# Optimization experiments

Hardware: AMD Instinct MI355X
Metric: run time of the kernel (lower is better)

## Reference

```python
import jax, jax.numpy as jnp
import numpy as np

B, T, D, H, W = 2, 16, 32, 64, 64
C2 = 2 * D          # channels after real/imag concat
E4 = 4 * C2         # para_pool expand=4
EPS = 1e-5


def _cnorm(z, g, b):
    # complex 'norm': LayerNorm over concat([real, imag], -1), then recombine
    zc = jnp.concatenate([z.real, z.imag], axis=-1)
    mu = zc.mean(-1, keepdims=True)
    var = zc.var(-1, keepdims=True)
    zn = (zc - mu) / jnp.sqrt(var + EPS) * g + b
    r, i = jnp.split(zn, 2, axis=-1)
    return r + 1j * i


def setup_inputs() -> dict:
    key = jax.random.key(0)
    ks = jax.random.split(key, 16)
    f = jnp.float32
    sd = 1.0 / np.sqrt(D)
    return {
        "x_real": jax.random.normal(ks[0], (B, T, D, H, W), f),
        "x_imag": jax.random.normal(ks[1], (B, T, D, H, W), f),
        "dt": jnp.ones((1,), f),
        "ln_s_g": jnp.ones((C2,), f), "ln_s_b": jnp.zeros((C2,), f),
        "conv_w": jax.random.normal(ks[2], (3, 3, C2, C2), f) * 0.05,
        "conv_b": jnp.zeros((C2,), f),
        "spec_fr": jax.random.normal(ks[3], (H, W, D), f) * 0.1,
        "spec_fi": jax.random.normal(ks[4], (H, W, D), f) * 0.1,
        "lam_r": -jnp.abs(jax.random.normal(ks[5], (D,), f)) * 0.5,
        "lam_i": jax.random.normal(ks[6], (D,), f),
        "E_r": jax.random.normal(ks[7], (D, D), f) * sd,
        "E_i": jax.random.normal(ks[8], (D, D), f) * sd,
        "Dm_r": jax.random.normal(ks[9], (D, D), f) * sd,
        "Dm_i": jax.random.normal(ks[10], (D, D), f) * sd,
        "ln_t_g": jnp.ones((C2,), f), "ln_t_b": jnp.zeros((C2,), f),
        "pool_w1": jax.random.normal(ks[11], (E4, C2), f) * 0.05,
        "pool_b1": jnp.zeros((E4,), f),
        "pool_w2": jax.random.normal(ks[12], (C2, E4), f) * 0.05,
        "pool_b2": jnp.zeros((C2,), f),
        "gate": jnp.full((1,), 0.5, f),
    }


def reference(x_real, x_imag, dt, ln_s_g, ln_s_b, conv_w, conv_b, spec_fr, spec_fi,
              lam_r, lam_i, E_r, E_i, Dm_r, Dm_i, ln_t_g, ln_t_b,
              pool_w1, pool_b1, pool_w2, pool_b2, gate):
    # work in channel-last layout [B,T,H,W,D]
    x = (x_real + 1j * x_imag).transpose(0, 1, 3, 4, 2)

    # ---- spatial block ----
    resid = x
    zn = _cnorm(x, ln_s_g, ln_s_b)                       # [B,T,H,W,D] complex
    zc = jnp.concatenate([zn.real, zn.imag], -1).reshape(B * T, H, W, C2)
    oc = jax.lax.conv_general_dilated(
        zc, conv_w, (1, 1), 'SAME',
        dimension_numbers=('NHWC', 'HWIO', 'NHWC')) + conv_b
    r, i = jnp.split(oc.reshape(B, T, H, W, C2), 2, axis=-1)
    cliff = r + 1j * i
    filt = spec_fr + 1j * spec_fi                         # [H,W,D]
    spec = jnp.fft.ifft2(jnp.fft.fft2(zn, axes=(2, 3)) * filt, axes=(2, 3))
    g = gate[0]
    x = g * cliff + (1.0 - g) * spec + resid

    # ---- temporal block: eigen-encode -> linear-decay scan -> decode ----
    resid = x
    xt = _cnorm(x.transpose(0, 2, 3, 1, 4).reshape(B * H * W, T, D), ln_t_g, ln_t_b)
    lam = lam_r + 1j * lam_i
    dts = dt[0]
    op_decay = jnp.exp(lam * dts)                         # [D]
    op_forcing = (jnp.exp(lam * dts) - 1.0) / lam          # [D] (exact ZOH forcing)
    Em = E_r + 1j * E_i
    Dm = Dm_r + 1j * Dm_i
    x_eig = jnp.einsum('ntd,de->nte', xt, Em)
    u = x_eig * op_forcing                                # [BHW,T,D]
    a = jnp.broadcast_to(op_decay, u.shape).astype(u.dtype)

    def comb(c1, c2):
        a1, u1 = c1
        a2, u2 = c2
        return (a1 * a2, u1 * a2 + u2)

    h = jax.lax.associative_scan(comb, (a, u), axis=1)[1]  # h_t = a_t h_{t-1} + u_t
    xo = jnp.einsum('ntd,de->nte', h, Dm).real
    x_drift = xo.reshape(B, H, W, T, D).transpose(0, 3, 1, 2, 4)
    x = x_drift + resid

    # ---- para pool (pointwise channel MLP on concat(real, imag)) ----
    resid = x
    xp = jnp.concatenate([x.real, x.imag], -1)            # [B,T,H,W,2D]
    y = jax.nn.gelu(jnp.einsum('bthwc,ec->bthwe', xp, pool_w1) + pool_b1)
    y = jnp.einsum('bthwe,ce->bthwc', y, pool_w2) + pool_b2
    r, i = jnp.split(y, 2, axis=-1)
    x = (r + 1j * i) + resid

    return x.transpose(0, 1, 4, 2, 3)                     # [B,T,D,H,W] complex
```

## Files before the change

kernel.cpp:

```cpp
#include <hip/hip_runtime.h>
#include <cstddef>


#define EPS_ 1e-5f
#define PI_  3.14159265358979323846f
#define ND_  4194304ull

typedef __attribute__((ext_vector_type(8))) short bf16x8;
typedef __attribute__((ext_vector_type(4))) float f32x4;

__device__ __forceinline__ short f2bf(float f) {
  unsigned u = __float_as_uint(f);
  unsigned r = (u + 0x7fffu + ((u >> 16) & 1u)) >> 16;
  return (short)r;
}
__device__ __forceinline__ float bf2f(short h) {
  return __uint_as_float(((unsigned)(unsigned short)h) << 16);
}

__global__ __launch_bounds__(256) void k0_prepw(
    const float* __restrict__ wgt, unsigned short* __restrict__ wb) {
  int j = blockIdx.x * 256 + threadIdx.x;
  int kk = j >> 12;
  int rem = j & 4095;
  int oc = rem >> 6;
  int ic = rem & 63;
  wb[j] = (unsigned short)f2bf(wgt[((size_t)kk * 64 + ic) * 64 + oc]);
}

__global__ __launch_bounds__(256) void k8_pool_prepw(
    const float* __restrict__ pw1, const float* __restrict__ pw2,
    const float* __restrict__ Er, const float* __restrict__ Ei,
    const float* __restrict__ Dmr, const float* __restrict__ Dmi,
    unsigned short* __restrict__ pwb1, unsigned short* __restrict__ pwb2,
    unsigned short* __restrict__ eB, unsigned short* __restrict__ dB) {
  int j = blockIdx.x * 256 + threadIdx.x;
  if (j < 16384) {
    pwb1[j] = (unsigned short)f2bf(pw1[j]);
  } else if (j < 32768) {
    int j2 = j - 16384;
    int ec = j2 >> 12;
    int rem = j2 & 4095;
    int oc = rem >> 6;
    int el = rem & 63;
    pwb2[j2] = (unsigned short)f2bf(pw2[(size_t)oc * 256 + ec * 64 + el]);
  } else if (j < 36864) {
    int j2 = j - 32768;
    int col = j2 >> 6, k = j2 & 63;
    float v;
    if (col < 32) {
      v = (k < 32) ? Er[k * 32 + col] : -Ei[(k - 32) * 32 + col];
    } else {
      int e = col - 32;
      v = (k < 32) ? Ei[k * 32 + e] : Er[(k - 32) * 32 + e];
    }
    eB[j2] = (unsigned short)f2bf(v);
  } else if (j < 38912) {
    int j2 = j - 36864;
    int e2 = j2 >> 6, k = j2 & 63;
    float v = (k < 32) ? Dmr[k * 32 + e2] : -Dmi[(k - 32) * 32 + e2];
    dB[j2] = (unsigned short)f2bf(v);
  }
}

__global__ __launch_bounds__(256) void k1_cnorm_spatial(
    const float* __restrict__ xr, const float* __restrict__ xi,
    const float* __restrict__ g, const float* __restrict__ b,
    float* __restrict__ znr, float* __restrict__ zni,
    unsigned short* __restrict__ znb) {
  int tok = blockIdx.x * 256 + threadIdx.x;
  int bt = tok >> 12;
  int hw = tok & 4095;
  const float* pr = xr + (size_t)bt * 131072 + hw;
  const float* pi = xi + (size_t)bt * 131072 + hw;
  float r[32], q[32];
  float s = 0.f;
#pragma unroll
  for (int d = 0; d < 32; d++) {
    r[d] = pr[(size_t)d * 4096];
    q[d] = pi[(size_t)d * 4096];
    s += r[d] + q[d];
  }
  float mu = s * 0.015625f;
  float v = 0.f;
#pragma unroll
  for (int d = 0; d < 32; d++) {
    float a = r[d] - mu, c = q[d] - mu;
    v += a * a + c * c;
  }
  float rstd = rsqrtf(v * 0.015625f + EPS_);
#pragma unroll
  for (int d = 0; d < 32; d++) {
    r[d] = (r[d] - mu) * rstd * g[d] + b[d];
    q[d] = (q[d] - mu) * rstd * g[32 + d] + b[32 + d];
  }
  float4* outr = (float4*)(znr + (size_t)tok * 32);
  float4* outi = (float4*)(zni + (size_t)tok * 32);
#pragma unroll
  for (int j = 0; j < 8; j++) {
    outr[j] = make_float4(r[4 * j], r[4 * j + 1], r[4 * j + 2], r[4 * j + 3]);
    outi[j] = make_float4(q[4 * j], q[4 * j + 1], q[4 * j + 2], q[4 * j + 3]);
  }
  short* zb = (short*)(znb + (size_t)tok * 64);
#pragma unroll
  for (int j = 0; j < 4; j++) {
    bf16x8 vr, vq;
#pragma unroll
    for (int k = 0; k < 8; k++) {
      vr[k] = f2bf(r[8 * j + k]);
      vq[k] = f2bf(q[8 * j + k]);
    }
    *(bf16x8*)(zb + 8 * j) = vr;
    *(bf16x8*)(zb + 32 + 8 * j) = vq;
  }
}

__global__ __launch_bounds__(256) void k2_conv(
    const unsigned short* __restrict__ znb, const unsigned short* __restrict__ wb,
    const float* __restrict__ bias,
    float* __restrict__ clr, float* __restrict__ cli) {
  __shared__ __align__(16) short sA[3 * 66 * 88];
  __shared__ __align__(16) short sW[2][64 * 72];
  int h = blockIdx.x, bt = blockIdx.y;
  for (int v = threadIdx.x; v < 1584; v += 256) {
    int c0 = (v & 7) * 8;
    int row = v >> 3;
    int wp = row % 66;
    int rr = row / 66;
    int hh = h + rr - 1;
    int w = wp - 1;
    bf16x8 val = {0, 0, 0, 0, 0, 0, 0, 0};
    if ((unsigned)hh < 64u && (unsigned)w < 64u) {
      int tok = (bt * 64 + hh) * 64 + w;
      val = *(const bf16x8*)(znb + (size_t)tok * 64 + c0);
    }
    *(bf16x8*)(&sA[(rr * 66 + wp) * 88 + c0]) = val;
  }
  for (int v = threadIdx.x; v < 512; v += 256) {
    int oc = v >> 3, ic0 = (v & 7) * 8;
    *(bf16x8*)(&sW[0][oc * 72 + ic0]) = *(const bf16x8*)(wb + v * 8);
  }
  int lane = threadIdx.x & 63;
  int wv = threadIdx.x >> 6;
  int m0 = wv * 16;
  int lr = lane & 15;
  int quad = lane >> 4;
  f32x4 acc[4];
#pragma unroll
  for (int nt = 0; nt < 4; nt++) {
    float bz = bias[nt * 16 + lr];
    acc[nt][0] = bz; acc[nt][1] = bz; acc[nt][2] = bz; acc[nt][3] = bz;
  }
  __syncthreads();
  for (int kk = 0; kk < 9; kk++) {
    int cur = kk & 1;
    if (kk < 8) {
      const unsigned short* src = wb + (size_t)(kk + 1) * 4096;
      for (int v = threadIdx.x; v < 512; v += 256) {
        int oc = v >> 3, ic0 = (v & 7) * 8;
        *(bf16x8*)(&sW[cur ^ 1][oc * 72 + ic0]) = *(const bf16x8*)(src + v * 8);
      }
    }
    int kh = kk / 3, kw = kk - kh * 3;
    const short* arow = &sA[((size_t)kh * 66 + (m0 + lr + kw)) * 88 + quad * 8];
#pragma unroll
    for (int ks = 0; ks < 2; ks++) {
      bf16x8 afrag = *(const bf16x8*)(arow + ks * 32);
#pragma unroll
      for (int nt = 0; nt < 4; nt++) {
        bf16x8 bfrag = *(const bf16x8*)&sW[cur][(size_t)(nt * 16 + lr) * 72 + ks * 32 + quad * 8];
        acc[nt] = __builtin_amdgcn_mfma_f32_16x16x32_bf16(afrag, bfrag, acc[nt], 0, 0, 0);
      }
    }
    __syncthreads();
  }
  int tokbase = (bt * 64 + h) * 64 + m0;
#pragma unroll
  for (int nt = 0; nt < 4; nt++) {
    int oc = nt * 16 + lr;
    float* dst = (oc < 32) ? (clr + oc) : (cli + (oc - 32));
#pragma unroll
    for (int reg = 0; reg < 4; reg++) {
      int m = quad * 4 + reg;
      dst[(size_t)(tokbase + m) * 32] = acc[nt][reg];
    }
  }
}

__global__ __launch_bounds__(256) void k3_dftw(
    const float* __restrict__ znr, const float* __restrict__ zni,
    float* __restrict__ fqr, float* __restrict__ fqi) {
  __shared__ __align__(16) short sX[64 * 72];
  __shared__ float twr[64], twi[64];
  int h = blockIdx.x, bt = blockIdx.y;
  size_t base = (size_t)((bt * 64 + h) * 64) * 32;
  if (threadIdx.x < 64) {
    float ang = -2.f * PI_ * (float)threadIdx.x * (1.f / 64.f);
    twr[threadIdx.x] = cosf(ang);
    twi[threadIdx.x] = sinf(ang);
  }
  for (int i = threadIdx.x; i < 2048; i += 256) {
    int w = i >> 5, d = i & 31;
    sX[d * 72 + w] = f2bf(znr[base + i]);
    sX[(d + 32) * 72 + w] = f2bf(zni[base + i]);
  }
  __syncthreads();
  int lane = threadIdx.x & 63;
  int wv = threadIdx.x >> 6;
  int m0 = wv * 16;
  int lr = lane & 15;
  int quad = lane >> 4;
  int r = m0 + lr;
  bf16x8 tr0, tr1, ti0, ti1;
#pragma unroll
  for (int j = 0; j < 8; j++) {
    int i0 = (r * (quad * 8 + j)) & 63;
    int i1 = (r * (quad * 8 + j + 32)) & 63;
    tr0[j] = f2bf(twr[i0]); ti0[j] = f2bf(twi[i0]);
    tr1[j] = f2bf(twr[i1]); ti1[j] = f2bf(twi[i1]);
  }
  f32x4 p1[4], p2[4];
#pragma unroll
  for (int nt = 0; nt < 4; nt++) {
    p1[nt][0] = 0.f; p1[nt][1] = 0.f; p1[nt][2] = 0.f; p1[nt][3] = 0.f;
    p2[nt][0] = 0.f; p2[nt][1] = 0.f; p2[nt][2] = 0.f; p2[nt][3] = 0.f;
  }
#pragma unroll
  for (int ks = 0; ks < 2; ks++) {
    bf16x8 tr = ks ? tr1 : tr0;
    bf16x8 ti = ks ? ti1 : ti0;
#pragma unroll
    for (int nt = 0; nt < 4; nt++) {
      bf16x8 xh = *(const bf16x8*)&sX[(size_t)(nt * 16 + lr) * 72 + ks * 32 + quad * 8];
      p1[nt] = __builtin_amdgcn_mfma_f32_16x16x32_bf16(tr, xh, p1[nt], 0, 0, 0);
      p2[nt] = __builtin_amdgcn_mfma_f32_16x16x32_bf16(ti, xh, p2[nt], 0, 0, 0);
    }
  }
#pragma unroll
  for (int nt = 0; nt < 2; nt++) {
#pragma unroll
    for (int reg = 0; reg < 4; reg++) {
      int k = m0 + quad * 4 + reg;
      int d = nt * 16 + lr;
      float Or = p1[nt][reg] - p2[nt + 2][reg];
      float Oi = p1[nt + 2][reg] + p2[nt][reg];
      size_t la = base + (size_t)k * 32 + d;
      fqr[la] = Or;
      fqi[la] = Oi;
    }
  }
}

__global__ __launch_bounds__(256) void k4_dfth(
    float* __restrict__ fqr, float* __restrict__ fqi,
    const float* __restrict__ flr, const float* __restrict__ fli) {
  __shared__ __align__(16) short sX[64 * 72];
  __shared__ float twr[64], twi[64];
  int kw = blockIdx.x, bt = blockIdx.y;
  if (threadIdx.x < 64) {
    float ang = -2.f * PI_ * (float)threadIdx.x * (1.f / 64.f);
    twr[threadIdx.x] = cosf(ang);
    twi[threadIdx.x] = sinf(ang);
  }
  for (int i = threadIdx.x; i < 2048; i += 256) {
    int hh = i >> 5, d = i & 31;
    size_t ga = (size_t)((bt * 64 + hh) * 64 + kw) * 32 + d;
    sX[d * 72 + hh] = f2bf(fqr[ga]);
    sX[(d + 32) * 72 + hh] = f2bf(fqi[ga]);
  }
  __syncthreads();
  int lane = threadIdx.x & 63;
  int wv = threadIdx.x >> 6;
  int m0 = wv * 16;
  int lr = lane & 15;
  int quad = lane >> 4;
  int r = m0 + lr;
  bf16x8 tr0, tr1, ti0, ti1;
#pragma unroll
  for (int j = 0; j < 8; j++) {
    int i0 = (r * (quad * 8 + j)) & 63;
    int i1 = (r * (quad * 8 + j + 32)) & 63;
    tr0[j] = f2bf(twr[i0]); ti0[j] = f2bf(twi[i0]);
    tr1[j] = f2bf(twr[i1]); ti1[j] = f2bf(twi[i1]);
  }
  f32x4 p1[4], p2[4];
#pragma unroll
  for (int nt = 0; nt < 4; nt++) {
    p1[nt][0] = 0.f; p1[nt][1] = 0.f; p1[nt][2] = 0.f; p1[nt][3] = 0.f;
    p2[nt][0] = 0.f; p2[nt][1] = 0.f; p2[nt][2] = 0.f; p2[nt][3] = 0.f;
  }
#pragma unroll
  for (int ks = 0; ks < 2; ks++) {
    bf16x8 tr = ks ? tr1 : tr0;
    bf16x8 ti = ks ? ti1 : ti0;
#pragma unroll
    for (int nt = 0; nt < 4; nt++) {
      bf16x8 xh = *(const bf16x8*)&sX[(size_t)(nt * 16 + lr) * 72 + ks * 32 + quad * 8];
      p1[nt] = __builtin_amdgcn_mfma_f32_16x16x32_bf16(tr, xh, p1[nt], 0, 0, 0);
      p2[nt] = __builtin_amdgcn_mfma_f32_16x16x32_bf16(ti, xh, p2[nt], 0, 0, 0);
    }
  }
  __syncthreads();
#pragma unroll
  for (int nt = 0; nt < 2; nt++) {
#pragma unroll
    for (int reg = 0; reg < 4; reg++) {
      int kh = m0 + quad * 4 + reg;
      int d = nt * 16 + lr;
      float Or = p1[nt][reg] - p2[nt + 2][reg];
      float Oi = p1[nt + 2][reg] + p2[nt][reg];
      size_t fa = (size_t)(kh * 64 + kw) * 32 + d;
      float fr = flr[fa], fi = fli[fa];
      float pr = Or * fr - Oi * fi;
      float pi = Or * fi + Oi * fr;
      sX[d * 72 + kh] = f2bf(pr);
      sX[(d + 32) * 72 + kh] = f2bf(pi);
    }
  }
  __syncthreads();
#pragma unroll
  for (int nt = 0; nt < 4; nt++) {
    p1[nt][0] = 0.f; p1[nt][1] = 0.f; p1[nt][2] = 0.f; p1[nt][3] = 0.f;
    p2[nt][0] = 0.f; p2[nt][1] = 0.f; p2[nt][2] = 0.f; p2[nt][3] = 0.f;
  }
#pragma unroll
  for (int ks = 0; ks < 2; ks++) {
    bf16x8 tr = ks ? tr1 : tr0;
    bf16x8 ti = ks ? ti1 : ti0;
#pragma unroll
    for (int nt = 0; nt < 4; nt++) {
      bf16x8 xh = *(const bf16x8*)&sX[(size_t)(nt * 16 + lr) * 72 + ks * 32 + quad * 8];
      p1[nt] = __builtin_amdgcn_mfma_f32_16x16x32_bf16(tr, xh, p1[nt], 0, 0, 0);
      p2[nt] = __builtin_amdgcn_mfma_f32_16x16x32_bf16(ti, xh, p2[nt], 0, 0, 0);
    }
  }
#pragma unroll
  for (int nt = 0; nt < 2; nt++) {
#pragma unroll
    for (int reg = 0; reg < 4; reg++) {
      int hh = m0 + quad * 4 + reg;
      int d = nt * 16 + lr;
      float Or = (p1[nt][reg] + p2[nt + 2][reg]) * 0.015625f;
      float Oi = (p1[nt + 2][reg] - p2[nt][reg]) * 0.015625f;
      size_t ga = (size_t)((bt * 64 + hh) * 64 + kw) * 32 + d;
      fqr[ga] = Or;
      fqi[ga] = Oi;
    }
  }
}

__global__ __launch_bounds__(256) void k5_idftw_combine(
    const float* __restrict__ fqr, const float* __restrict__ fqi,
    const float* __restrict__ clr, const float* __restrict__ cli,
    const float* __restrict__ xr_in, const float* __restrict__ xi_in,
    const float* __restrict__ gate,
    float* __restrict__ xr, float* __restrict__ xi) {
  __shared__ __align__(16) short sX[64 * 72];
  __shared__ float twr[64], twi[64];
  int h = blockIdx.x, bt = blockIdx.y;
  size_t base = (size_t)((bt * 64 + h) * 64) * 32;
  if (threadIdx.x < 64) {
    float ang = -2.f * PI_ * (float)threadIdx.x * (1.f / 64.f);
    twr[threadIdx.x] = cosf(ang);
    twi[threadIdx.x] = sinf(ang);
  }
  for (int i = threadIdx.x; i < 2048; i += 256) {
    int kw = i >> 5, d = i & 31;
    sX[d * 72 + kw] = f2bf(fqr[base + i]);
    sX[(d + 32) * 72 + kw] = f2bf(fqi[base + i]);
  }
  __syncthreads();
  int lane = threadIdx.x & 63;
  int wv = threadIdx.x >> 6;
  int m0 = wv * 16;
  int lr = lane & 15;
  int quad = lane >> 4;
  int r = m0 + lr;
  bf16x8 tr0, tr1, ti0, ti1;
#pragma unroll
  for (int j = 0; j < 8; j++) {
    int i0 = (r * (quad * 8 + j)) & 63;
    int i1 = (r * (quad * 8 + j + 32)) & 63;
    tr0[j] = f2bf(twr[i0]); ti0[j] = f2bf(twi[i0]);
    tr1[j] = f2bf(twr[i1]); ti1[j] = f2bf(twi[i1]);
  }
  f32x4 p1[4], p2[4];
#pragma unroll
  for (int nt = 0; nt < 4; nt++) {
    p1[nt][0] = 0.f; p1[nt][1] = 0.f; p1[nt][2] = 0.f; p1[nt][3] = 0.f;
    p2[nt][0] = 0.f; p2[nt][1] = 0.f; p2[nt][2] = 0.f; p2[nt][3] = 0.f;
  }
#pragma unroll
  for (int ks = 0; ks < 2; ks++) {
    bf16x8 tr = ks ? tr1 : tr0;
    bf16x8 ti = ks ? ti1 : ti0;
#pragma unroll
    for (int nt = 0; nt < 4; nt++) {
      bf16x8 xh = *(const bf16x8*)&sX[(size_t)(nt * 16 + lr) * 72 + ks * 32 + quad * 8];
      p1[nt] = __builtin_amdgcn_mfma_f32_16x16x32_bf16(tr, xh, p1[nt], 0, 0, 0);
      p2[nt] = __builtin_amdgcn_mfma_f32_16x16x32_bf16(ti, xh, p2[nt], 0, 0, 0);
    }
  }
  float g = gate[0];
  float gi = 1.f - g;
#pragma unroll
  for (int nt = 0; nt < 2; nt++) {
#pragma unroll
    for (int reg = 0; reg < 4; reg++) {
      int w = m0 + quad * 4 + reg;
      int d = nt * 16 + lr;
      float Or = (p1[nt][reg] + p2[nt + 2][reg]) * 0.015625f;
      float Oi = (p1[nt + 2][reg] - p2[nt][reg]) * 0.015625f;
      size_t la = base + (size_t)w * 32 + d;
      size_t ga = (size_t)(bt * 32 + d) * 4096 + h * 64 + w;
      xr[la] = g * clr[la] + gi * Or + xr_in[ga];
      xi[la] = g * cli[la] + gi * Oi + xi_in[ga];
    }
  }
}

__global__ __launch_bounds__(256) void k6_temporal(
    float* __restrict__ xr, float* __restrict__ xi,
    const float* __restrict__ lamr, const float* __restrict__ lami,
    const unsigned short* __restrict__ eB, const unsigned short* __restrict__ dB,
    const float* __restrict__ lg, const float* __restrict__ lb,
    const float* __restrict__ dtp) {
  __shared__ __align__(16) short sAh[128 * 72];
  __shared__ __align__(16) short sAl[128 * 72];
  __shared__ __align__(16) short sBe[64 * 72];
  __shared__ __align__(16) short sBd[32 * 72];
  int n0 = blockIdx.x * 8;
  for (int v = threadIdx.x; v < 768; v += 256) {
    int c0 = (v & 7) * 8;
    if (v < 512) {
      *(bf16x8*)(&sBe[(v >> 3) * 72 + c0]) = *(const bf16x8*)(eB + v * 8);
    } else {
      int v2 = v - 512;
      *(bf16x8*)(&sBd[(v2 >> 3) * 72 + c0]) = *(const bf16x8*)(dB + v2 * 8);
    }
  }
  if (threadIdx.x < 128) {
    int sIc = threadIdx.x >> 4;
    int t = threadIdx.x & 15;
    int n = n0 + sIc;
    int bb = n >> 12;
    int hw = n & 4095;
    size_t tokb = ((size_t)(bb * 16 + t)) * 4096 + hw;
    const float4* pr = (const float4*)(xr + tokb * 32);
    const float4* pi = (const float4*)(xi + tokb * 32);
    float rv[32], iv[32];
    float s = 0.f;
#pragma unroll
    for (int j = 0; j < 8; j++) {
      float4 a = pr[j];
      float4 c = pi[j];
      rv[4 * j] = a.x; rv[4 * j + 1] = a.y; rv[4 * j + 2] = a.z; rv[4 * j + 3] = a.w;
      iv[4 * j] = c.x; iv[4 * j + 1] = c.y; iv[4 * j + 2] = c.z; iv[4 * j + 3] = c.w;
      s += a.x + a.y + a.z + a.w + c.x + c.y + c.z + c.w;
    }
    float mu = s * 0.015625f;
    float v = 0.f;
#pragma unroll
    for (int d = 0; d < 32; d++) {
      float a = rv[d] - mu, c = iv[d] - mu;
      v += a * a + c * c;
    }
    float rstd = rsqrtf(v * 0.015625f + EPS_);
    int row = threadIdx.x * 72;
#pragma unroll
    for (int j = 0; j < 4; j++) {
      bf16x8 vh, vl, wh, wl;
#pragma unroll
      for (int k = 0; k < 8; k++) {
        float a = (rv[8 * j + k] - mu) * rstd * lg[8 * j + k] + lb[8 * j + k];
        float c = (iv[8 * j + k] - mu) * rstd * lg[32 + 8 * j + k] + lb[32 + 8 * j + k];
        short ah = f2bf(a);
        vh[k] = ah; vl[k] = f2bf(a - bf2f(ah));
        short ch = f2bf(c);
        wh[k] = ch; wl[k] = f2bf(c - bf2f(ch));
      }
      *(bf16x8*)(&sAh[row + 8 * j]) = vh;
      *(bf16x8*)(&sAl[row + 8 * j]) = vl;
      *(bf16x8*)(&sAh[row + 32 + 8 * j]) = wh;
      *(bf16x8*)(&sAl[row + 32 + 8 * j]) = wl;
    }
  }
  __syncthreads();
  int lane = threadIdx.x & 63;
  int wv = threadIdx.x >> 6;
  int lr = lane & 15;
  int quad = lane >> 4;
  f32x4 p[2][4];
#pragma unroll
  for (int m = 0; m < 2; m++)
#pragma unroll
    for (int nt = 0; nt < 4; nt++) {
      p[m][nt][0] = 0.f; p[m][nt][1] = 0.f; p[m][nt][2] = 0.f; p[m][nt][3] = 0.f;
    }
#pragma unroll
  for (int m = 0; m < 2; m++) {
    int rowA = ((2 * wv + m) * 16 + lr) * 72;
#pragma unroll
    for (int ks = 0; ks < 2; ks++) {
      bf16x8 ah = *(const bf16x8*)&sAh[rowA + ks * 32 + quad * 8];
      bf16x8 al = *(const bf16x8*)&sAl[rowA + ks * 32 + quad * 8];
#pragma unroll
      for (int nt = 0; nt < 4; nt++) {
        bf16x8 bfrag = *(const bf16x8*)&sBe[(nt * 16 + lr) * 72 + ks * 32 + quad * 8];
        p[m][nt] = __builtin_amdgcn_mfma_f32_16x16x32_bf16(ah, bfrag, p[m][nt], 0, 0, 0);
        p[m][nt] = __builtin_amdgcn_mfma_f32_16x16x32_bf16(al, bfrag, p[m][nt], 0, 0, 0);
      }
    }
  }
  float dts = dtp[0];
  float acr[2], aci[2], fcr[2], fci[2];
#pragma unroll
  for (int eo = 0; eo < 2; eo++) {
    int e = eo * 16 + lr;
    float lrr = lamr[e], lii = lami[e];
    float ex = expf(lrr * dts);
    float dcr = ex * cosf(lii * dts);
    float dci = ex * sinf(lii * dts);
    acr[eo] = dcr; aci[eo] = dci;
    float nr = dcr - 1.f, ni = dci;
    float invden = 1.f / (lrr * lrr + lii * lii);
    fcr[eo] = (nr * lrr + ni * lii) * invden;
    fci[eo] = (ni * lrr - nr * lii) * invden;
  }
#pragma unroll
  for (int m = 0; m < 2; m++) {
#pragma unroll
    for (int eo = 0; eo < 2; eo++) {
      float ar = acr[eo], ai_ = aci[eo];
      float fr = fcr[eo], fi = fci[eo];
      float a2r = ar * ar - ai_ * ai_, a2i = 2.f * ar * ai_;
      float a3r = a2r * ar - a2i * ai_, a3i = a2r * ai_ + a2i * ar;
      float a4r = a2r * a2r - a2i * a2i, a4i = 2.f * a2r * a2i;
      float a8r = a4r * a4r - a4i * a4i, a8i = 2.f * a4r * a4i;
      float apr[4] = {ar, a2r, a3r, a4r};
      float api[4] = {ai_, a2i, a3i, a4i};
      float hlr[4], hli[4];
#pragma unroll
      for (int reg = 0; reg < 4; reg++) {
        float xr_ = p[m][eo][reg], xi_ = p[m][2 + eo][reg];
        float ur = xr_ * fr - xi_ * fi;
        float ui = xr_ * fi + xi_ * fr;
        if (reg == 0) {
          hlr[0] = ur; hli[0] = ui;
        } else {
          float t1 = ar * hlr[reg - 1] - ai_ * hli[reg - 1] + ur;
          float t2 = ar * hli[reg - 1] + ai_ * hlr[reg - 1] + ui;
          hlr[reg] = t1; hli[reg] = t2;
        }
      }
      float Sr = hlr[3], Si = hli[3];
      float t1r = __shfl_up(Sr, 16), t1i = __shfl_up(Si, 16);
      if (quad >= 1) { Sr += a4r * t1r - a4i * t1i; Si += a4r * t1i + a4i * t1r; }
      float t2r = __shfl_up(Sr, 32), t2i = __shfl_up(Si, 32);
      if (quad >= 2) { Sr += a8r * t2r - a8i * t2i; Si += a8r * t2i + a8i * t2r; }
      float hinr = __shfl_up(Sr, 16), hini = __shfl_up(Si, 16);
      if (quad == 0) { hinr = 0.f; hini = 0.f; }
      int e = eo * 16 + lr;
#pragma unroll
      for (int reg = 0; reg < 4; reg++) {
        float hr_ = apr[reg] * hinr - api[reg] * hini + hlr[reg];
        float hi_ = apr[reg] * hini + api[reg] * hinr + hli[reg];
        int row = ((2 * wv + m) * 16 + quad * 4 + reg) * 72;
        short b1 = f2bf(hr_);
        sAh[row + e] = b1;
        sAl[row + e] = f2bf(hr_ - bf2f(b1));
        short b2 = f2bf(hi_);
        sAh[row + 32 + e] = b2;
        sAl[row + 32 + e] = f2bf(hi_ - bf2f(b2));
      }
    }
  }
  __syncthreads();
  f32x4 q[2][2];
#pragma unroll
  for (int m = 0; m < 2; m++)
#pragma unroll
    for (int nt = 0; nt < 2; nt++) {
      q[m][nt][0] = 0.f; q[m][nt][1] = 0.f; q[m][nt][2] = 0.f; q[m][nt][3] = 0.f;
    }
#pragma unroll
  for (int m = 0; m < 2; m++) {
    int rowA = ((2 * wv + m) * 16 + lr) * 72;
#pragma unroll
    for (int ks = 0; ks < 2; ks++) {
      bf16x8 ah = *(const bf16x8*)&sAh[rowA + ks * 32 + quad * 8];
      bf16x8 al = *(const bf16x8*)&sAl[rowA + ks * 32 + quad * 8];
#pragma unroll
      for (int nt = 0; nt < 2; nt++) {
        bf16x8 bfrag = *(const bf16x8*)&sBd[(nt * 16 + lr) * 72 + ks * 32 + quad * 8];
        q[m][nt] = __builtin_amdgcn_mfma_f32_16x16x32_bf16(ah, bfrag, q[m][nt], 0, 0, 0);
        q[m][nt] = __builtin_amdgcn_mfma_f32_16x16x32_bf16(al, bfrag, q[m][nt], 0, 0, 0);
      }
    }
  }
#pragma unroll
  for (int m = 0; m < 2; m++) {
    int n = n0 + 2 * wv + m;
    int bb = n >> 12;
    int hw = n & 4095;
#pragma unroll
    for (int nt = 0; nt < 2; nt++) {
      int e2 = nt * 16 + lr;
#pragma unroll
      for (int reg = 0; reg < 4; reg++) {
        int t = quad * 4 + reg;
        size_t tokb = ((size_t)(bb * 16 + t)) * 4096 + hw;
        xr[tokb * 32 + e2] += q[m][nt][reg];
      }
    }
  }
}

__global__ __launch_bounds__(256) void k7_pool(
    const float* __restrict__ xr, const float* __restrict__ xi,
    const unsigned short* __restrict__ pwb1, const float* __restrict__ pb1,
    const unsigned short* __restrict__ pwb2, const float* __restrict__ pb2,
    float* __restrict__ out, long long out_n) {
  __shared__ __align__(16) short sX[64 * 72];
  __shared__ __align__(16) short sH[64 * 72];
  __shared__ __align__(16) short sW1[64 * 72];
  __shared__ __align__(16) short sW2[64 * 72];
  int tok0 = blockIdx.x * 64;
  for (int i = threadIdx.x; i < 4096; i += 256) {
    int t = i >> 6, c = i & 63;
    float v = (c < 32) ? xr[(size_t)(tok0 + t) * 32 + c]
                       : xi[(size_t)(tok0 + t) * 32 + c - 32];
    sX[t * 72 + c] = f2bf(v);
  }
  int lane = threadIdx.x & 63;
  int wv = threadIdx.x >> 6;
  int lr = lane & 15;
  int quad = lane >> 4;
  int m0 = wv * 16;
  f32x4 acc2[4];
#pragma unroll
  for (int nt = 0; nt < 4; nt++) {
    float bz = pb2[nt * 16 + lr];
    acc2[nt][0] = bz; acc2[nt][1] = bz; acc2[nt][2] = bz; acc2[nt][3] = bz;
  }
  const short* arow = &sX[(size_t)(m0 + lr) * 72 + quad * 8];
  const short* hrow = &sH[(size_t)(m0 + lr) * 72 + quad * 8];
  for (int ec = 0; ec < 4; ec++) {
    __syncthreads();
    {
      const unsigned short* w1 = pwb1 + (size_t)ec * 4096;
      const unsigned short* w2 = pwb2 + (size_t)ec * 4096;
      for (int v = threadIdx.x; v < 512; v += 256) {
        int row = v >> 3, c0 = (v & 7) * 8;
        *(bf16x8*)(&sW1[row * 72 + c0]) = *(const bf16x8*)(w1 + v * 8);
        *(bf16x8*)(&sW2[row * 72 + c0]) = *(const bf16x8*)(w2 + v * 8);
      }
    }
    __syncthreads();
    f32x4 acc1[4];
#pragma unroll
    for (int nt = 0; nt < 4; nt++) {
      float bz = pb1[ec * 64 + nt * 16 + lr];
      acc1[nt][0] = bz; acc1[nt][1] = bz; acc1[nt][2] = bz; acc1[nt][3] = bz;
    }
#pragma unroll
    for (int ks = 0; ks < 2; ks++) {
      bf16x8 ah = *(const bf16x8*)(arow + ks * 32);
#pragma unroll
      for (int nt = 0; nt < 4; nt++) {
        bf16x8 bfrag = *(const bf16x8*)&sW1[(size_t)(nt * 16 + lr) * 72 + ks * 32 + quad * 8];
        acc1[nt] = __builtin_amdgcn_mfma_f32_16x16x32_bf16(ah, bfrag, acc1[nt], 0, 0, 0);
      }
    }
#pragma unroll
    for (int nt = 0; nt < 4; nt++) {
#pragma unroll
      for (int reg = 0; reg < 4; reg++) {
        float x = acc1[nt][reg];
        float u2 = 1.5957691216f * (x + 0.044715f * x * x * x);
        float e2 = __expf(u2);
        float gl = x - x * __builtin_amdgcn_rcpf(e2 + 1.f);
        sH[(m0 + quad * 4 + reg) * 72 + nt * 16 + lr] = f2bf(gl);
      }
    }
#pragma unroll
    for (int ks = 0; ks < 2; ks++) {
      bf16x8 af = *(const bf16x8*)(hrow + ks * 32);
#pragma unroll
      for (int nt = 0; nt < 4; nt++) {
        bf16x8 bfrag = *(const bf16x8*)&sW2[(size_t)(nt * 16 + lr) * 72 + ks * 32 + quad * 8];
        acc2[nt] = __builtin_amdgcn_mfma_f32_16x16x32_bf16(af, bfrag, acc2[nt], 0, 0, 0);
      }
    }
  }
#pragma unroll
  for (int nt = 0; nt < 4; nt++) {
    int oc = nt * 16 + lr;
#pragma unroll
    for (int reg = 0; reg < 4; reg++) {
      int t = tok0 + m0 + quad * 4 + reg;
      float resid = (oc < 32) ? xr[(size_t)t * 32 + oc] : xi[(size_t)t * 32 + oc - 32];
      float val = acc2[nt][reg] + resid;
      int bt = t >> 12;
      int hw = t & 4095;
      int d = (oc < 32) ? oc : oc - 32;
      size_t cidx = (size_t)(bt * 32 + d) * 4096 + hw;
      long long pos = (long long)cidx + ((oc < 32) ? 0ll : (long long)ND_);
      if (pos < out_n) out[pos] = val;
    }
  }
}

extern "C" void kernel_launch(void* const* d_in, const int* in_sizes, int n_in,
                              void* d_out, int out_size, void* d_ws, size_t ws_size,
                              hipStream_t stream) {
  (void)in_sizes; (void)n_in;
  const float* xr_in = (const float*)d_in[0];
  const float* xi_in = (const float*)d_in[1];
  const float* dt = (const float*)d_in[2];
  const float* ln_s_g = (const float*)d_in[3];
  const float* ln_s_b = (const float*)d_in[4];
  const float* conv_w = (const float*)d_in[5];
  const float* conv_b = (const float*)d_in[6];
  const float* spec_fr = (const float*)d_in[7];
  const float* spec_fi = (const float*)d_in[8];
  const float* lam_r = (const float*)d_in[9];
  const float* lam_i = (const float*)d_in[10];
  const float* E_r = (const float*)d_in[11];
  const float* E_i = (const float*)d_in[12];
  const float* Dm_r = (const float*)d_in[13];
  const float* Dm_i = (const float*)d_in[14];
  const float* ln_t_g = (const float*)d_in[15];
  const float* ln_t_b = (const float*)d_in[16];
  const float* pw1 = (const float*)d_in[17];
  const float* pb1 = (const float*)d_in[18];
  const float* pw2 = (const float*)d_in[19];
  const float* pb2 = (const float*)d_in[20];
  const float* gate = (const float*)d_in[21];

  if (ws_size < 6ull * ND_ * 4ull) return;

  float* ws = (float*)d_ws;
  float* znr = ws;
  float* zni = ws + ND_;
  float* clr = ws + 2 * ND_;
  float* cli = ws + 3 * ND_;
  float* fqr = ws + 4 * ND_;
  float* fqi = ws + 5 * ND_;
  float* out = (float*)d_out;
  unsigned short* znb = (unsigned short*)fqr;
  unsigned short* wb = (unsigned short*)fqi;
  unsigned short* pwb1 = (unsigned short*)fqr;
  unsigned short* pwb2 = pwb1 + 16384;
  unsigned short* eB = pwb1 + 32768;
  unsigned short* dB = pwb1 + 36864;

  k0_prepw<<<144, 256, 0, stream>>>(conv_w, wb);
  k1_cnorm_spatial<<<512, 256, 0, stream>>>(xr_in, xi_in, ln_s_g, ln_s_b, znr, zni, znb);
  k2_conv<<<dim3(64, 32), 256, 0, stream>>>(znb, wb, conv_b, clr, cli);
  k3_dftw<<<dim3(64, 32), 256, 0, stream>>>(znr, zni, fqr, fqi);
  k4_dfth<<<dim3(64, 32), 256, 0, stream>>>(fqr, fqi, spec_fr, spec_fi);
  k5_idftw_combine<<<dim3(64, 32), 256, 0, stream>>>(fqr, fqi, clr, cli, xr_in, xi_in,
                                                     gate, znr, zni);
  k8_pool_prepw<<<156, 256, 0, stream>>>(pw1, pw2, E_r, E_i, Dm_r, Dm_i,
                                         pwb1, pwb2, eB, dB);
  k6_temporal<<<1024, 256, 0, stream>>>(znr, zni, lam_r, lam_i, eB, dB,
                                        ln_t_g, ln_t_b, dt);
  k7_pool<<<2048, 256, 0, stream>>>(znr, zni, pwb1, pb1, pwb2, pb2, out, (long long)out_size);
}
```

Baseline: 288.3 us.

## Fuse spatial cnorm with W-axis DFT and drop split-bf16 in temporal block

The spatial layernorm kernel now writes its normalized tokens as bf16 straight into shared memory and runs the W-direction DFT on four rows per block. This removes the separate DFT-W kernel and the fp32 round trip of znr/zni through global memory. Separately, the temporal kernel no longer splits activations into high and low bf16 parts, which halves its MFMA count and shared-memory use but lowers precision of the eigenbasis projections. Workspace aliasing is shuffled so the bf16 buffers reuse znr/zni.

```diff
diff --git a/kernel.cpp b/kernel.cpp
--- a/kernel.cpp
+++ b/kernel.cpp
@@ -63,14 +63,22 @@
   }
 }
 
-__global__ __launch_bounds__(256) void k1_cnorm_spatial(
+__global__ __launch_bounds__(256) void k13_cnorm_dftw(
     const float* __restrict__ xr, const float* __restrict__ xi,
     const float* __restrict__ g, const float* __restrict__ b,
-    float* __restrict__ znr, float* __restrict__ zni,
-    unsigned short* __restrict__ znb) {
-  int tok = blockIdx.x * 256 + threadIdx.x;
+    unsigned short* __restrict__ znb,
+    float* __restrict__ fqr, float* __restrict__ fqi) {
+  __shared__ __align__(16) short sX[4][64 * 72];
+  __shared__ float twr[64], twi[64];
+  int tid = threadIdx.x;
+  int tok = blockIdx.x * 256 + tid;
   int bt = tok >> 12;
   int hw = tok & 4095;
+  if (tid < 64) {
+    float ang = -2.f * PI_ * (float)tid * (1.f / 64.f);
+    twr[tid] = cosf(ang);
+    twi[tid] = sinf(ang);
+  }
   const float* pr = xr + (size_t)bt * 131072 + hw;
   const float* pi = xi + (size_t)bt * 131072 + hw;
   float r[32], q[32];
@@ -89,29 +97,74 @@
     v += a * a + c * c;
   }
   float rstd = rsqrtf(v * 0.015625f + EPS_);
-#pragma unroll
-  for (int d = 0; d < 32; d++) {
-    r[d] = (r[d] - mu) * rstd * g[d] + b[d];
-    q[d] = (q[d] - mu) * rstd * g[32 + d] + b[32 + d];
-  }
-  float4* outr = (float4*)(znr + (size_t)tok * 32);
-  float4* outi = (float4*)(zni + (size_t)tok * 32);
-#pragma unroll
-  for (int j = 0; j < 8; j++) {
-    outr[j] = make_float4(r[4 * j], r[4 * j + 1], r[4 * j + 2], r[4 * j + 3]);
-    outi[j] = make_float4(q[4 * j], q[4 * j + 1], q[4 * j + 2], q[4 * j + 3]);
-  }
+  int rr = tid >> 6;
+  int w = tid & 63;
   short* zb = (short*)(znb + (size_t)tok * 64);
+  short* sxp = &sX[rr][0];
 #pragma unroll
   for (int j = 0; j < 4; j++) {
     bf16x8 vr, vq;
 #pragma unroll
     for (int k = 0; k < 8; k++) {
-      vr[k] = f2bf(r[8 * j + k]);
-      vq[k] = f2bf(q[8 * j + k]);
+      int d = 8 * j + k;
+      float a = (r[d] - mu) * rstd * g[d] + b[d];
+      float c = (q[d] - mu) * rstd * g[32 + d] + b[32 + d];
+      short ba = f2bf(a);
+      short bc = f2bf(c);
+      vr[k] = ba; vq[k] = bc;
+      sxp[d * 72 + w] = ba;
+      sxp[(d + 32) * 72 + w] = bc;
     }
     *(bf16x8*)(zb + 8 * j) = vr;
     *(bf16x8*)(zb + 32 + 8 * j) = vq;
+  }
+  __syncthreads();
+  int lane = tid & 63;
+  int wv = tid >> 6;
+  int m0 = wv * 16;
+  int lr = lane & 15;
+  int quad = lane >> 4;
+  int rk = m0 + lr;
+  bf16x8 tr0, tr1, ti0, ti1;
+#pragma unroll
+  for (int j = 0; j < 8; j++) {
+    int i0 = (rk * (quad * 8 + j)) & 63;
+    int i1 = (rk * (quad * 8 + j + 32)) & 63;
+    tr0[j] = f2bf(twr[i0]); ti0[j] = f2bf(twi[i0]);
+    tr1[j] = f2bf(twr[i1]); ti1[j] = f2bf(twi[i1]);
+  }
+  for (int row = 0; row < 4; row++) {
+    f32x4 p1[4], p2[4];
+#pragma unroll
+    for (int nt = 0; nt < 4; nt++) {
+      p1[nt][0] = 0.f; p1[nt][1] = 0.f; p1[nt][2] = 0.f; p1[nt][3] = 0.f;
+      p2[nt][0] = 0.f; p2[nt][1] = 0.f; p2[nt][2] = 0.f; p2[nt][3] = 0.f;
+    }
+#pragma unroll
+    for (int ks = 0; ks < 2; ks++) {
+      bf16x8 tr = ks ? tr1 : tr0;
+      bf16x8 ti = ks ? ti1 : ti0;
+#pragma unroll
+      for (int nt = 0; nt < 4; nt++) {
+        bf16x8 xh = *(const bf16x8*)&sX[row][(size_t)(nt * 16 + lr) * 72 + ks * 32 + quad * 8];
+        p1[nt] = __builtin_amdgcn_mfma_f32_16x16x32_bf16(tr, xh, p1[nt], 0, 0, 0);
+        p2[nt] = __builtin_amdgcn_mfma_f32_16x16x32_bf16(ti, xh, p2[nt], 0, 0, 0);
+      }
+    }
+    size_t base = (size_t)(blockIdx.x * 256 + row * 64) * 32;
+#pragma unroll
+    for (int nt = 0; nt < 2; nt++) {
+#pragma unroll
+      for (int reg = 0; reg < 4; reg++) {
+        int k = m0 + quad * 4 + reg;
+        int d = nt * 16 + lr;
+        float Or = p1[nt][reg] - p2[nt + 2][reg];
+        float Oi = p1[nt + 2][reg] + p2[nt][reg];
+        size_t la = base + (size_t)k * 32 + d;
+        fqr[la] = Or;
+        fqi[la] = Oi;
+      }
+    }
   }
 }
 
@@ -187,70 +240,6 @@
   }
 }
 
-__global__ __launch_bounds__(256) void k3_dftw(
-    const float* __restrict__ znr, const float* __restrict__ zni,
-    float* __restrict__ fqr, float* __restrict__ fqi) {
-  __shared__ __align__(16) short sX[64 * 72];
-  __shared__ float twr[64], twi[64];
-  int h = blockIdx.x, bt = blockIdx.y;
-  size_t base = (size_t)((bt * 64 + h) * 64) * 32;
-  if (threadIdx.x < 64) {
-    float ang = -2.f * PI_ * (float)threadIdx.x * (1.f / 64.f);
-    twr[threadIdx.x] = cosf(ang);
-    twi[threadIdx.x] = sinf(ang);
-  }
-  for (int i = threadIdx.x; i < 2048; i += 256) {
-    int w = i >> 5, d = i & 31;
-    sX[d * 72 + w] = f2bf(znr[base + i]);
-    sX[(d + 32) * 72 + w] = f2bf(zni[base + i]);
-  }
-  __syncthreads();
-  int lane = threadIdx.x & 63;
-  int wv = threadIdx.x >> 6;
-  int m0 = wv * 16;
-  int lr = lane & 15;
-  int quad = lane >> 4;
-  int r = m0 + lr;
-  bf16x8 tr0, tr1, ti0, ti1;
-#pragma unroll
-  for (int j = 0; j < 8; j++) {
-    int i0 = (r * (quad * 8 + j)) & 63;
-    int i1 = (r * (quad * 8 + j + 32)) & 63;
-    tr0[j] = f2bf(twr[i0]); ti0[j] = f2bf(twi[i0]);
-    tr1[j] = f2bf(twr[i1]); ti1[j] = f2bf(twi[i1]);
-  }
-  f32x4 p1[4], p2[4];
-#pragma unroll
-  for (int nt = 0; nt < 4; nt++) {
-    p1[nt][0] = 0.f; p1[nt][1] = 0.f; p1[nt][2] = 0.f; p1[nt][3] = 0.f;
-    p2[nt][0] = 0.f; p2[nt][1] = 0.f; p2[nt][2] = 0.f; p2[nt][3] = 0.f;
-  }
-#pragma unroll
-  for (int ks = 0; ks < 2; ks++) {
-    bf16x8 tr = ks ? tr1 : tr0;
-    bf16x8 ti = ks ? ti1 : ti0;
-#pragma unroll
-    for (int nt = 0; nt < 4; nt++) {
-      bf16x8 xh = *(const bf16x8*)&sX[(size_t)(nt * 16 + lr) * 72 + ks * 32 + quad * 8];
-      p1[nt] = __builtin_amdgcn_mfma_f32_16x16x32_bf16(tr, xh, p1[nt], 0, 0, 0);
-      p2[nt] = __builtin_amdgcn_mfma_f32_16x16x32_bf16(ti, xh, p2[nt], 0, 0, 0);
-    }
-  }
-#pragma unroll
-  for (int nt = 0; nt < 2; nt++) {
-#pragma unroll
-    for (int reg = 0; reg < 4; reg++) {
-      int k = m0 + quad * 4 + reg;
-      int d = nt * 16 + lr;
-      float Or = p1[nt][reg] - p2[nt + 2][reg];
-      float Oi = p1[nt + 2][reg] + p2[nt][reg];
-      size_t la = base + (size_t)k * 32 + d;
-      fqr[la] = Or;
-      fqi[la] = Oi;
-    }
-  }
-}
-
 __global__ __launch_bounds__(256) void k4_dfth(
     float* __restrict__ fqr, float* __restrict__ fqi,
     const float* __restrict__ flr, const float* __restrict__ fli) {
@@ -425,8 +414,7 @@
     const unsigned short* __restrict__ eB, const unsigned short* __restrict__ dB,
     const float* __restrict__ lg, const float* __restrict__ lb,
     const float* __restrict__ dtp) {
-  __shared__ __align__(16) short sAh[128 * 72];
-  __shared__ __align__(16) short sAl[128 * 72];
+  __shared__ __align__(16) short sA[128 * 72];
   __shared__ __align__(16) short sBe[64 * 72];
   __shared__ __align__(16) short sBd[32 * 72];
   int n0 = blockIdx.x * 8;
@@ -469,20 +457,16 @@
     int row = threadIdx.x * 72;
 #pragma unroll
     for (int j = 0; j < 4; j++) {
-      bf16x8 vh, vl, wh, wl;
+      bf16x8 vh, wh;
 #pragma unroll
       for (int k = 0; k < 8; k++) {
         float a = (rv[8 * j + k] - mu) * rstd * lg[8 * j + k] + lb[8 * j + k];
         float c = (iv[8 * j + k] - mu) * rstd * lg[32 + 8 * j + k] + lb[32 + 8 * j + k];
-        short ah = f2bf(a);
-        vh[k] = ah; vl[k] = f2bf(a - bf2f(ah));
-        short ch = f2bf(c);
-        wh[k] = ch; wl[k] = f2bf(c - bf2f(ch));
-      }
-      *(bf16x8*)(&sAh[row + 8 * j]) = vh;
-      *(bf16x8*)(&sAl[row + 8 * j]) = vl;
-      *(bf16x8*)(&sAh[row + 32 + 8 * j]) = wh;
-      *(bf16x8*)(&sAl[row + 32 + 8 * j]) = wl;
+        vh[k] = f2bf(a);
+        wh[k] = f2bf(c);
+      }
+      *(bf16x8*)(&sA[row + 8 * j]) = vh;
+      *(bf16x8*)(&sA[row + 32 + 8 * j]) = wh;
     }
   }
   __syncthreads();
@@ -502,13 +486,11 @@
     int rowA = ((2 * wv + m) * 16 + lr) * 72;
 #pragma unroll
     for (int ks = 0; ks < 2; ks++) {
-      bf16x8 ah = *(const bf16x8*)&sAh[rowA + ks * 32 + quad * 8];
-      bf16x8 al = *(const bf16x8*)&sAl[rowA + ks * 32 + quad * 8];
+      bf16x8 ah = *(const bf16x8*)&sA[rowA + ks * 32 + quad * 8];
 #pragma unroll
       for (int nt = 0; nt < 4; nt++) {
         bf16x8 bfrag = *(const bf16x8*)&sBe[(nt * 16 + lr) * 72 + ks * 32 + quad * 8];
         p[m][nt] = __builtin_amdgcn_mfma_f32_16x16x32_bf16(ah, bfrag, p[m][nt], 0, 0, 0);
-        p[m][nt] = __builtin_amdgcn_mfma_f32_16x16x32_bf16(al, bfrag, p[m][nt], 0, 0, 0);
       }
     }
   }
@@ -566,12 +548,8 @@
         float hr_ = apr[reg] * hinr - api[reg] * hini + hlr[reg];
         float hi_ = apr[reg] * hini + api[reg] * hinr + hli[reg];
         int row = ((2 * wv + m) * 16 + quad * 4 + reg) * 72;
-        short b1 = f2bf(hr_);
-        sAh[row + e] = b1;
-        sAl[row + e] = f2bf(hr_ - bf2f(b1));
-        short b2 = f2bf(hi_);
-        sAh[row + 32 + e] = b2;
-        sAl[row + 32 + e] = f2bf(hi_ - bf2f(b2));
+        sA[row + e] = f2bf(hr_);
+        sA[row + 32 + e] = f2bf(hi_);
       }
     }
   }
@@ -588,13 +566,11 @@
     int rowA = ((2 * wv + m) * 16 + lr) * 72;
 #pragma unroll
     for (int ks = 0; ks < 2; ks++) {
-      bf16x8 ah = *(const bf16x8*)&sAh[rowA + ks * 32 + quad * 8];
-      bf16x8 al = *(const bf16x8*)&sAl[rowA + ks * 32 + quad * 8];
+      bf16x8 ah = *(const bf16x8*)&sA[rowA + ks * 32 + quad * 8];
 #pragma unroll
       for (int nt = 0; nt < 2; nt++) {
         bf16x8 bfrag = *(const bf16x8*)&sBd[(nt * 16 + lr) * 72 + ks * 32 + quad * 8];
         q[m][nt] = __builtin_amdgcn_mfma_f32_16x16x32_bf16(ah, bfrag, q[m][nt], 0, 0, 0);
-        q[m][nt] = __builtin_amdgcn_mfma_f32_16x16x32_bf16(al, bfrag, q[m][nt], 0, 0, 0);
       }
     }
   }
@@ -748,17 +724,16 @@
   float* fqr = ws + 4 * ND_;
   float* fqi = ws + 5 * ND_;
   float* out = (float*)d_out;
-  unsigned short* znb = (unsigned short*)fqr;
-  unsigned short* wb = (unsigned short*)fqi;
+  unsigned short* znb = (unsigned short*)znr;
+  unsigned short* wb = (unsigned short*)zni;
   unsigned short* pwb1 = (unsigned short*)fqr;
   unsigned short* pwb2 = pwb1 + 16384;
   unsigned short* eB = pwb1 + 32768;
   unsigned short* dB = pwb1 + 36864;
 
   k0_prepw<<<144, 256, 0, stream>>>(conv_w, wb);
-  k1_cnorm_spatial<<<512, 256, 0, stream>>>(xr_in, xi_in, ln_s_g, ln_s_b, znr, zni, znb);
+  k13_cnorm_dftw<<<512, 256, 0, stream>>>(xr_in, xi_in, ln_s_g, ln_s_b, znb, fqr, fqi);
   k2_conv<<<dim3(64, 32), 256, 0, stream>>>(znb, wb, conv_b, clr, cli);
-  k3_dftw<<<dim3(64, 32), 256, 0, stream>>>(znr, zni, fqr, fqi);
   k4_dfth<<<dim3(64, 32), 256, 0, stream>>>(fqr, fqi, spec_fr, spec_fi);
   k5_idftw_combine<<<dim3(64, 32), 256, 0, stream>>>(fqr, fqi, clr, cli, xr_in, xi_in,
                                                      gate, znr, zni);
```

After: 259.1 us. -10.1%, faster.
